# Kernel optimization log

Measured on AMD Instinct MI355X. Metric: run time of the kernel, lower is better.

The kernel has to match this reference:

```python
import jax, jax.numpy as jnp
import numpy as np

N = 50000      # nodes
E = 625000     # edges
IN = 128       # in_dim
H = 8          # num_heads
D = 16         # out_dim (per head)
SCALE = np.sqrt(D).astype(np.float32)


def setup_inputs() -> dict:
    key = jax.random.key(0)
    ks = jax.random.split(key, 12)
    init = 1.0 / np.sqrt(IN)
    return {
        "h": jax.random.normal(ks[0], (N, IN), jnp.float32),
        "e": jax.random.normal(ks[1], (E, IN), jnp.float32),
        "src": jax.random.randint(ks[2], (E,), 0, N, jnp.int32),
        "dst": jax.random.randint(ks[3], (E,), 0, N, jnp.int32),
        "Wq": jax.random.normal(ks[4], (IN, H * D), jnp.float32) * init,
        "bq": jnp.zeros((H * D,), jnp.float32),
        "Wk": jax.random.normal(ks[5], (IN, H * D), jnp.float32) * init,
        "bk": jnp.zeros((H * D,), jnp.float32),
        "Wv": jax.random.normal(ks[6], (IN, H * D), jnp.float32) * init,
        "bv": jnp.zeros((H * D,), jnp.float32),
        "We": jax.random.normal(ks[7], (IN, H * D), jnp.float32) * init,
        "be": jnp.zeros((H * D,), jnp.float32),
    }


def reference(h, e, src, dst, Wq, bq, Wk, bk, Wv, bv, We, be):
    # Node / edge projections, reshaped to [*, H, D]
    Q = (h @ Wq + bq).reshape(N, H, D)
    K = (h @ Wk + bk).reshape(N, H, D)
    V = (h @ Wv + bv).reshape(N, H, D)
    pe = (e @ We + be).reshape(E, H, D)

    # Edge-wise: score = (K[src] * Q[dst]) / sqrt(D) * proj_e   [E, H, D]
    score = (K[src] * Q[dst]) / SCALE * pe
    e_out = score  # out_edge_features('score') captured before exp

    # exp(clamp(sum_d score, -5, 5))  -> [E, H, 1]
    s = jnp.exp(jnp.clip(jnp.sum(score, axis=-1, keepdims=True), -5.0, 5.0))

    # scatter-sum over destination nodes
    wV = jax.ops.segment_sum(V[src] * s, dst, num_segments=N)  # [N, H, D]
    z = jax.ops.segment_sum(s, dst, num_segments=N)            # [N, H, 1]

    h_out = wV / (z + 1e-6)
    return h_out, e_out
```

## Files before the change

kernel.cpp:

```cpp
#include <hip/hip_runtime.h>

#define Nn 50000
#define Ee 625000
#define INDIM 128
#define NH 8
#define HDIM 16

typedef __attribute__((ext_vector_type(8))) short short8;
typedef __attribute__((ext_vector_type(4))) float floatx4;

#define LDS_STRIDE 136

__device__ inline unsigned short f2bf(float f) {
    unsigned u = __builtin_bit_cast(unsigned, f);
    u = (u + 0x7FFFu + ((u >> 16) & 1u)) >> 16;
    return (unsigned short)u;
}

__device__ inline void stage_tile_bf16(const float* __restrict__ g, long row0, long nrows_total,
                                       unsigned short* lds, int tid) {
    for (int it = 0; it < 16; ++it) {
        int r = it * 8 + (tid >> 5);
        int c4 = (tid & 31) * 4;
        float4 v = make_float4(0.f, 0.f, 0.f, 0.f);
        long gr = row0 + r;
        if (gr < nrows_total) {
            v = *reinterpret_cast<const float4*>(g + gr * 128 + c4);
        }
        ushort4 o;
        o.x = f2bf(v.x); o.y = f2bf(v.y); o.z = f2bf(v.z); o.w = f2bf(v.w);
        *reinterpret_cast<ushort4*>(lds + r * LDS_STRIDE + c4) = o;
    }
}

__device__ inline void stage_w_t(const float* __restrict__ W, unsigned short* lds, int tid) {
    for (int it = 0; it < 64; ++it) {
        int idx = it * 256 + tid;
        int k = idx >> 7, n = idx & 127;
        lds[n * LDS_STRIDE + k] = f2bf(W[idx]);
    }
}

__global__ __launch_bounds__(256) void node_qkv(
    const float* __restrict__ h,
    const float* __restrict__ Wq, const float* __restrict__ bq,
    const float* __restrict__ Wk, const float* __restrict__ bk,
    const float* __restrict__ Wv, const float* __restrict__ bv,
    float* __restrict__ Q, float* __restrict__ K, float* __restrict__ V) {
    __shared__ unsigned short ht[128 * LDS_STRIDE];
    __shared__ unsigned short wt[128 * LDS_STRIDE];
    int tid = threadIdx.x;
    long n0 = (long)blockIdx.x * 128;
    stage_tile_bf16(h, n0, Nn, ht, tid);
    __syncthreads();

    int wave = tid >> 6, lane = tid & 63;
    int q4 = lane >> 4, col = lane & 15;

    short8 afr[2][4];
    for (int t = 0; t < 2; ++t) {
        int mrow = (wave * 2 + t) * 16 + col;
        for (int kc = 0; kc < 4; ++kc)
            afr[t][kc] = *reinterpret_cast<const short8*>(&ht[mrow * LDS_STRIDE + kc * 32 + q4 * 8]);
    }

    const float* Wm[3] = {Wq, Wk, Wv};
    const float* bm[3] = {bq, bk, bv};
    float* Om[3] = {Q, K, V};

    for (int mat = 0; mat < 3; ++mat) {
        __syncthreads();
        stage_w_t(Wm[mat], wt, tid);
        __syncthreads();
        for (int n = 0; n < 8; ++n) {
            short8 bfr[4];
            for (int kc = 0; kc < 4; ++kc)
                bfr[kc] = *reinterpret_cast<const short8*>(&wt[(n * 16 + col) * LDS_STRIDE + kc * 32 + q4 * 8]);
            float bias = bm[mat][n * 16 + col];
            for (int t = 0; t < 2; ++t) {
                floatx4 acc = {0.f, 0.f, 0.f, 0.f};
                for (int kc = 0; kc < 4; ++kc)
                    acc = __builtin_amdgcn_mfma_f32_16x16x32_bf16(afr[t][kc], bfr[kc], acc, 0, 0, 0);
                for (int r = 0; r < 4; ++r) {
                    long node = n0 + (wave * 2 + t) * 16 + q4 * 4 + r;
                    if (node < Nn) Om[mat][node * 128 + n * 16 + col] = acc[r] + bias;
                }
            }
        }
    }
}

__global__ __launch_bounds__(256) void edge_fused(
    const float* __restrict__ e, const int* __restrict__ src, const int* __restrict__ dst,
    const float* __restrict__ We, const float* __restrict__ be,
    const float* __restrict__ Q, const float* __restrict__ K, const float* __restrict__ V,
    float* __restrict__ e_out, float* __restrict__ hacc, float* __restrict__ z) {
    __shared__ unsigned short et[128 * LDS_STRIDE];
    __shared__ unsigned short wt[128 * LDS_STRIDE];
    __shared__ int ssrc[128];
    __shared__ int sdst[128];
    int tid = threadIdx.x;
    long e0 = (long)blockIdx.x * 128;
    stage_tile_bf16(e, e0, Ee, et, tid);
    stage_w_t(We, wt, tid);
    if (tid < 128) {
        long ge = e0 + tid;
        ssrc[tid] = (ge < Ee) ? src[ge] : 0;
        sdst[tid] = (ge < Ee) ? dst[ge] : 0;
    }
    __syncthreads();

    int wave = tid >> 6, lane = tid & 63;
    int q4 = lane >> 4, col = lane & 15;

    short8 afr[2][4];
    for (int t = 0; t < 2; ++t) {
        int mrow = (wave * 2 + t) * 16 + col;
        for (int kc = 0; kc < 4; ++kc)
            afr[t][kc] = *reinterpret_cast<const short8*>(&et[mrow * LDS_STRIDE + kc * 32 + q4 * 8]);
    }

    for (int head = 0; head < 8; ++head) {
        short8 bfr[4];
        for (int kc = 0; kc < 4; ++kc)
            bfr[kc] = *reinterpret_cast<const short8*>(&wt[(head * 16 + col) * LDS_STRIDE + kc * 32 + q4 * 8]);
        int hoff = head * 16 + col;
        float bias = be[hoff];
        for (int t = 0; t < 2; ++t) {
            floatx4 acc = {0.f, 0.f, 0.f, 0.f};
            for (int kc = 0; kc < 4; ++kc)
                acc = __builtin_amdgcn_mfma_f32_16x16x32_bf16(afr[t][kc], bfr[kc], acc, 0, 0, 0);
            int mt = wave * 2 + t;
            for (int r = 0; r < 4; ++r) {
                int el = mt * 16 + q4 * 4 + r;
                long ge = e0 + el;
                bool valid = ge < Ee;
                int s32 = ssrc[el], d32 = sdst[el];
                float pe = acc[r] + bias;
                float kv = K[s32 * 128 + hoff];
                float qv = Q[d32 * 128 + hoff];
                float score = kv * qv * 0.25f * pe;
                if (valid) e_out[ge * 128 + hoff] = score;
                float sum = score;
                sum += __shfl_xor(sum, 1, 16);
                sum += __shfl_xor(sum, 2, 16);
                sum += __shfl_xor(sum, 4, 16);
                sum += __shfl_xor(sum, 8, 16);
                float sval = __expf(fminf(fmaxf(sum, -5.0f), 5.0f));
                if (valid) {
                    float vv = V[s32 * 128 + hoff];
                    atomicAdd(&hacc[d32 * 128 + hoff], vv * sval);
                    if (col == 0) atomicAdd(&z[d32 * 8 + head], sval);
                }
            }
        }
    }
}

__global__ __launch_bounds__(256) void finalize(float* __restrict__ hacc, const float* __restrict__ z) {
    int i = blockIdx.x * 256 + threadIdx.x;
    int base = i * 4;
    if (base < Nn * 128) {
        float4 a = *reinterpret_cast<float4*>(&hacc[base]);
        int node = base >> 7;
        int head = (base >> 4) & 7;
        float inv = 1.0f / (z[node * 8 + head] + 1e-6f);
        a.x *= inv; a.y *= inv; a.z *= inv; a.w *= inv;
        *reinterpret_cast<float4*>(&hacc[base]) = a;
    }
}

extern "C" void kernel_launch(void* const* d_in, const int* in_sizes, int n_in,
                              void* d_out, int out_size, void* d_ws, size_t ws_size,
                              hipStream_t stream) {
    const float* h  = (const float*)d_in[0];
    const float* e  = (const float*)d_in[1];
    const int*   src = (const int*)d_in[2];
    const int*   dst = (const int*)d_in[3];
    const float* Wq = (const float*)d_in[4];  const float* bq = (const float*)d_in[5];
    const float* Wk = (const float*)d_in[6];  const float* bk = (const float*)d_in[7];
    const float* Wv = (const float*)d_in[8];  const float* bv = (const float*)d_in[9];
    const float* We = (const float*)d_in[10]; const float* be = (const float*)d_in[11];

    float* out  = (float*)d_out;
    float* hout = out;
    float* eout = out + (size_t)Nn * 128;

    float* ws = (float*)d_ws;
    float* Q = ws;
    float* K = ws + (size_t)Nn * 128;
    float* V = ws + 2 * (size_t)Nn * 128;
    float* z = ws + 3 * (size_t)Nn * 128;

    hipMemsetAsync(hout, 0, (size_t)Nn * 128 * sizeof(float), stream);
    hipMemsetAsync(z, 0, (size_t)Nn * NH * sizeof(float), stream);

    node_qkv<<<(Nn + 127) / 128, 256, 0, stream>>>(h, Wq, bq, Wk, bk, Wv, bv, Q, K, V);
    edge_fused<<<(Ee + 127) / 128, 256, 0, stream>>>(e, src, dst, We, be, Q, K, V, eout, hout, z);
    finalize<<<(Nn * 128 / 4 + 255) / 256, 256, 0, stream>>>(hout, z);
}
```

Before: 1.314 ms.

## Drop LDS staging, load MFMA fragments from global, split QKV across grid

Both the node projection and edge kernels stop staging tiles and transposed weights into 70KB of shared memory. They now build bf16 MFMA fragments directly from global loads, with strided weight reads served from cache. This removes the LDS occupancy limit and the barriers, allowing more resident blocks (launch bounds set to 4 per SM). The edge kernel also keeps src/dst indices in registers and processes two heads per iteration so the K/Q/V gathers can overlap. The QKV kernel is split over a second grid dimension, one matrix per block. The cost is redundant uncoalesced weight reads per wave.

New measurement: 1.248 ms. 1.05x faster.

```diff
diff --git a/kernel.cpp b/kernel.cpp
--- a/kernel.cpp
+++ b/kernel.cpp
@@ -9,148 +9,172 @@
 typedef __attribute__((ext_vector_type(8))) short short8;
 typedef __attribute__((ext_vector_type(4))) float floatx4;
 
-#define LDS_STRIDE 136
-
 __device__ inline unsigned short f2bf(float f) {
     unsigned u = __builtin_bit_cast(unsigned, f);
     u = (u + 0x7FFFu + ((u >> 16) & 1u)) >> 16;
     return (unsigned short)u;
 }
 
-__device__ inline void stage_tile_bf16(const float* __restrict__ g, long row0, long nrows_total,
-                                       unsigned short* lds, int tid) {
-    for (int it = 0; it < 16; ++it) {
-        int r = it * 8 + (tid >> 5);
-        int c4 = (tid & 31) * 4;
-        float4 v = make_float4(0.f, 0.f, 0.f, 0.f);
-        long gr = row0 + r;
-        if (gr < nrows_total) {
-            v = *reinterpret_cast<const float4*>(g + gr * 128 + c4);
-        }
-        ushort4 o;
-        o.x = f2bf(v.x); o.y = f2bf(v.y); o.z = f2bf(v.z); o.w = f2bf(v.w);
-        *reinterpret_cast<ushort4*>(lds + r * LDS_STRIDE + c4) = o;
-    }
-}
-
-__device__ inline void stage_w_t(const float* __restrict__ W, unsigned short* lds, int tid) {
-    for (int it = 0; it < 64; ++it) {
-        int idx = it * 256 + tid;
-        int k = idx >> 7, n = idx & 127;
-        lds[n * LDS_STRIDE + k] = f2bf(W[idx]);
-    }
-}
-
-__global__ __launch_bounds__(256) void node_qkv(
+__device__ inline short8 cvt8(float4 a, float4 b) {
+    short8 o;
+    o[0] = (short)f2bf(a.x); o[1] = (short)f2bf(a.y);
+    o[2] = (short)f2bf(a.z); o[3] = (short)f2bf(a.w);
+    o[4] = (short)f2bf(b.x); o[5] = (short)f2bf(b.y);
+    o[6] = (short)f2bf(b.z); o[7] = (short)f2bf(b.w);
+    return o;
+}
+
+__device__ inline short8 wfrag(const float* __restrict__ W, int n, int k0) {
+    short8 o;
+#pragma unroll
+    for (int j = 0; j < 8; ++j) o[j] = (short)f2bf(W[(size_t)(k0 + j) * 128 + n]);
+    return o;
+}
+
+__global__ __launch_bounds__(256, 4) void node_qkv(
     const float* __restrict__ h,
     const float* __restrict__ Wq, const float* __restrict__ bq,
     const float* __restrict__ Wk, const float* __restrict__ bk,
     const float* __restrict__ Wv, const float* __restrict__ bv,
     float* __restrict__ Q, float* __restrict__ K, float* __restrict__ V) {
-    __shared__ unsigned short ht[128 * LDS_STRIDE];
-    __shared__ unsigned short wt[128 * LDS_STRIDE];
     int tid = threadIdx.x;
-    long n0 = (long)blockIdx.x * 128;
-    stage_tile_bf16(h, n0, Nn, ht, tid);
-    __syncthreads();
-
     int wave = tid >> 6, lane = tid & 63;
     int q4 = lane >> 4, col = lane & 15;
+    long n0 = (long)blockIdx.x * 128;
+    int mat = blockIdx.y;
+    const float* W = (mat == 0) ? Wq : (mat == 1) ? Wk : Wv;
+    const float* b = (mat == 0) ? bq : (mat == 1) ? bk : bv;
+    float*       O = (mat == 0) ? Q  : (mat == 1) ? K  : V;
 
     short8 afr[2][4];
+#pragma unroll
     for (int t = 0; t < 2; ++t) {
-        int mrow = (wave * 2 + t) * 16 + col;
-        for (int kc = 0; kc < 4; ++kc)
-            afr[t][kc] = *reinterpret_cast<const short8*>(&ht[mrow * LDS_STRIDE + kc * 32 + q4 * 8]);
-    }
-
-    const float* Wm[3] = {Wq, Wk, Wv};
-    const float* bm[3] = {bq, bk, bv};
-    float* Om[3] = {Q, K, V};
-
-    for (int mat = 0; mat < 3; ++mat) {
-        __syncthreads();
-        stage_w_t(Wm[mat], wt, tid);
-        __syncthreads();
-        for (int n = 0; n < 8; ++n) {
-            short8 bfr[4];
+        long row = n0 + (wave * 2 + t) * 16 + col;
+        bool v = row < Nn;
+        const float* p = h + row * 128 + q4 * 8;
+#pragma unroll
+        for (int kc = 0; kc < 4; ++kc) {
+            float4 x = make_float4(0.f, 0.f, 0.f, 0.f);
+            float4 y = make_float4(0.f, 0.f, 0.f, 0.f);
+            if (v) {
+                x = *reinterpret_cast<const float4*>(p + kc * 32);
+                y = *reinterpret_cast<const float4*>(p + kc * 32 + 4);
+            }
+            afr[t][kc] = cvt8(x, y);
+        }
+    }
+
+    for (int n = 0; n < 8; ++n) {
+        short8 bfr[4];
+#pragma unroll
+        for (int kc = 0; kc < 4; ++kc) bfr[kc] = wfrag(W, n * 16 + col, kc * 32 + q4 * 8);
+        float bias = b[n * 16 + col];
+#pragma unroll
+        for (int t = 0; t < 2; ++t) {
+            floatx4 acc = {0.f, 0.f, 0.f, 0.f};
+#pragma unroll
             for (int kc = 0; kc < 4; ++kc)
-                bfr[kc] = *reinterpret_cast<const short8*>(&wt[(n * 16 + col) * LDS_STRIDE + kc * 32 + q4 * 8]);
-            float bias = bm[mat][n * 16 + col];
-            for (int t = 0; t < 2; ++t) {
-                floatx4 acc = {0.f, 0.f, 0.f, 0.f};
-                for (int kc = 0; kc < 4; ++kc)
-                    acc = __builtin_amdgcn_mfma_f32_16x16x32_bf16(afr[t][kc], bfr[kc], acc, 0, 0, 0);
-                for (int r = 0; r < 4; ++r) {
-                    long node = n0 + (wave * 2 + t) * 16 + q4 * 4 + r;
-                    if (node < Nn) Om[mat][node * 128 + n * 16 + col] = acc[r] + bias;
-                }
-            }
-        }
-    }
-}
-
-__global__ __launch_bounds__(256) void edge_fused(
+                acc = __builtin_amdgcn_mfma_f32_16x16x32_bf16(afr[t][kc], bfr[kc], acc, 0, 0, 0);
+#pragma unroll
+            for (int r = 0; r < 4; ++r) {
+                long node = n0 + (wave * 2 + t) * 16 + q4 * 4 + r;
+                if (node < Nn) O[node * 128 + n * 16 + col] = acc[r] + bias;
+            }
+        }
+    }
+}
+
+__global__ __launch_bounds__(256, 4) void edge_fused(
     const float* __restrict__ e, const int* __restrict__ src, const int* __restrict__ dst,
     const float* __restrict__ We, const float* __restrict__ be,
     const float* __restrict__ Q, const float* __restrict__ K, const float* __restrict__ V,
     float* __restrict__ e_out, float* __restrict__ hacc, float* __restrict__ z) {
-    __shared__ unsigned short et[128 * LDS_STRIDE];
-    __shared__ unsigned short wt[128 * LDS_STRIDE];
-    __shared__ int ssrc[128];
-    __shared__ int sdst[128];
     int tid = threadIdx.x;
-    long e0 = (long)blockIdx.x * 128;
-    stage_tile_bf16(e, e0, Ee, et, tid);
-    stage_w_t(We, wt, tid);
-    if (tid < 128) {
-        long ge = e0 + tid;
-        ssrc[tid] = (ge < Ee) ? src[ge] : 0;
-        sdst[tid] = (ge < Ee) ? dst[ge] : 0;
-    }
-    __syncthreads();
-
     int wave = tid >> 6, lane = tid & 63;
     int q4 = lane >> 4, col = lane & 15;
+    long e0 = (long)blockIdx.x * 128;
 
     short8 afr[2][4];
+#pragma unroll
     for (int t = 0; t < 2; ++t) {
-        int mrow = (wave * 2 + t) * 16 + col;
-        for (int kc = 0; kc < 4; ++kc)
-            afr[t][kc] = *reinterpret_cast<const short8*>(&et[mrow * LDS_STRIDE + kc * 32 + q4 * 8]);
-    }
-
-    for (int head = 0; head < 8; ++head) {
-        short8 bfr[4];
-        for (int kc = 0; kc < 4; ++kc)
-            bfr[kc] = *reinterpret_cast<const short8*>(&wt[(head * 16 + col) * LDS_STRIDE + kc * 32 + q4 * 8]);
-        int hoff = head * 16 + col;
-        float bias = be[hoff];
+        long row = e0 + (wave * 2 + t) * 16 + col;
+        bool v = row < Ee;
+        const float* p = e + row * 128 + q4 * 8;
+#pragma unroll
+        for (int kc = 0; kc < 4; ++kc) {
+            float4 x = make_float4(0.f, 0.f, 0.f, 0.f);
+            float4 y = make_float4(0.f, 0.f, 0.f, 0.f);
+            if (v) {
+                x = *reinterpret_cast<const float4*>(p + kc * 32);
+                y = *reinterpret_cast<const float4*>(p + kc * 32 + 4);
+            }
+            afr[t][kc] = cvt8(x, y);
+        }
+    }
+
+    int sreg[2][4], dreg[2][4];
+#pragma unroll
+    for (int t = 0; t < 2; ++t)
+#pragma unroll
+        for (int r = 0; r < 4; ++r) {
+            long ge = e0 + (wave * 2 + t) * 16 + q4 * 4 + r;
+            bool v = ge < Ee;
+            sreg[t][r] = v ? src[ge] : 0;
+            dreg[t][r] = v ? dst[ge] : 0;
+        }
+
+#pragma unroll 1
+    for (int hg = 0; hg < 4; ++hg) {
+        floatx4 acc[2][2];
+        float bev[2];
+#pragma unroll
+        for (int hh = 0; hh < 2; ++hh) {
+            int head = hg * 2 + hh;
+            short8 bfr[4];
+#pragma unroll
+            for (int kc = 0; kc < 4; ++kc) bfr[kc] = wfrag(We, head * 16 + col, kc * 32 + q4 * 8);
+            bev[hh] = be[head * 16 + col];
+#pragma unroll
+            for (int t = 0; t < 2; ++t) {
+                floatx4 a = {0.f, 0.f, 0.f, 0.f};
+#pragma unroll
+                for (int kc = 0; kc < 4; ++kc)
+                    a = __builtin_amdgcn_mfma_f32_16x16x32_bf16(afr[t][kc], bfr[kc], a, 0, 0, 0);
+                acc[hh][t] = a;
+            }
+        }
+#pragma unroll
         for (int t = 0; t < 2; ++t) {
-            floatx4 acc = {0.f, 0.f, 0.f, 0.f};
-            for (int kc = 0; kc < 4; ++kc)
-                acc = __builtin_amdgcn_mfma_f32_16x16x32_bf16(afr[t][kc], bfr[kc], acc, 0, 0, 0);
-            int mt = wave * 2 + t;
+#pragma unroll
             for (int r = 0; r < 4; ++r) {
-                int el = mt * 16 + q4 * 4 + r;
-                long ge = e0 + el;
+                long ge = e0 + (wave * 2 + t) * 16 + q4 * 4 + r;
                 bool valid = ge < Ee;
-                int s32 = ssrc[el], d32 = sdst[el];
-                float pe = acc[r] + bias;
-                float kv = K[s32 * 128 + hoff];
-                float qv = Q[d32 * 128 + hoff];
-                float score = kv * qv * 0.25f * pe;
-                if (valid) e_out[ge * 128 + hoff] = score;
-                float sum = score;
-                sum += __shfl_xor(sum, 1, 16);
-                sum += __shfl_xor(sum, 2, 16);
-                sum += __shfl_xor(sum, 4, 16);
-                sum += __shfl_xor(sum, 8, 16);
-                float sval = __expf(fminf(fmaxf(sum, -5.0f), 5.0f));
-                if (valid) {
-                    float vv = V[s32 * 128 + hoff];
-                    atomicAdd(&hacc[d32 * 128 + hoff], vv * sval);
-                    if (col == 0) atomicAdd(&z[d32 * 8 + head], sval);
+                int s32 = sreg[t][r], d32 = dreg[t][r];
+                float kv[2], qv[2], vv[2];
+#pragma unroll
+                for (int hh = 0; hh < 2; ++hh) {
+                    int hoff = (hg * 2 + hh) * 16 + col;
+                    kv[hh] = K[(size_t)s32 * 128 + hoff];
+                    qv[hh] = Q[(size_t)d32 * 128 + hoff];
+                    vv[hh] = V[(size_t)s32 * 128 + hoff];
+                }
+#pragma unroll
+                for (int hh = 0; hh < 2; ++hh) {
+                    int head = hg * 2 + hh;
+                    int hoff = head * 16 + col;
+                    float pe = acc[hh][t][r] + bev[hh];
+                    float score = kv[hh] * qv[hh] * 0.25f * pe;
+                    if (valid) e_out[ge * 128 + hoff] = score;
+                    float sum = score;
+                    sum += __shfl_xor(sum, 1, 16);
+                    sum += __shfl_xor(sum, 2, 16);
+                    sum += __shfl_xor(sum, 4, 16);
+                    sum += __shfl_xor(sum, 8, 16);
+                    float sval = __expf(fminf(fmaxf(sum, -5.0f), 5.0f));
+                    if (valid) {
+                        atomicAdd(&hacc[(size_t)d32 * 128 + hoff], vv[hh] * sval);
+                        if (col == 0) atomicAdd(&z[(size_t)d32 * 8 + head], sval);
+                    }
                 }
             }
         }
@@ -195,7 +219,7 @@
     hipMemsetAsync(hout, 0, (size_t)Nn * 128 * sizeof(float), stream);
     hipMemsetAsync(z, 0, (size_t)Nn * NH * sizeof(float), stream);
 
-    node_qkv<<<(Nn + 127) / 128, 256, 0, stream>>>(h, Wq, bq, Wk, bk, Wv, bv, Q, K, V);
+    node_qkv<<<dim3((Nn + 127) / 128, 3), 256, 0, stream>>>(h, Wq, bq, Wk, bk, Wv, bv, Q, K, V);
     edge_fused<<<(Ee + 127) / 128, 256, 0, stream>>>(e, src, dst, We, be, Q, K, V, eout, hout, z);
     finalize<<<(Nn * 128 / 4 + 255) / 256, 256, 0, stream>>>(hout, z);
 }
```
